# Performance work log

Measured on AMD Instinct MI355X. Metric: run time of the kernel, lower is better.

The kernel has to match this reference:

```python
import jax, jax.numpy as jnp
import numpy as np

B, L, H, R = 8, 8256, 768, 24  # L = 128*129/2 flattened token-pair positions


def setup_inputs() -> dict:
    key = jax.random.key(0)
    k1, k2, k3 = jax.random.split(key, 3)
    hidden_state = jax.random.normal(k1, (B, L, H), dtype=jnp.float32)
    # per-relation Linear(hidden_size, 3) weights, stacked: (R, 3, H), (R, 3)
    W = jax.random.normal(k2, (R, 3, H), dtype=jnp.float32) * 0.02
    b = jax.random.normal(k3, (R, 3), dtype=jnp.float32) * 0.02
    return {"hidden_state": hidden_state, "W": W, "b": b}


def reference(hidden_state, W, b):
    # Batched equivalent of the per-relation Linear loop + stack(dim=1):
    # logits[b, r, l, t] = sum_h hidden_state[b,l,h] * W[r,t,h] + b[r,t]
    logits = jnp.einsum('blh,rth->brlt', hidden_state, W) + b[None, :, None, :]
    return jax.nn.softmax(logits, axis=-1)  # (B, R, L, 3)
```

## Files before the change

kernel.cpp:

```cpp
#include <hip/hip_runtime.h>
#include <hip/hip_bf16.h>


#define HD     768
#define LSEQ   8256
#define RREL   24
#define KSTEPS 24
#define NT     5
#define NCOL   72
#define MF     4

typedef float f32x4 __attribute__((ext_vector_type(4)));
typedef short s16x8 __attribute__((ext_vector_type(8)));
typedef int   i32x4 __attribute__((ext_vector_type(4)));

__device__ __forceinline__ unsigned f2bf_rne(float f) {
  unsigned u = __builtin_bit_cast(unsigned, f);
  u += 0x7FFFu + ((u >> 16) & 1u);
  return u >> 16;
}

__device__ __forceinline__ int pack2(float lo, float hi) {
  unsigned l = __bfloat16_as_ushort(__float2bfloat16(lo));
  unsigned h = __bfloat16_as_ushort(__float2bfloat16(hi));
  return (int)(l | (h << 16));
}

__global__ void conv_w_kernel(const float* __restrict__ W,
                              unsigned short* __restrict__ wsB) {
  int idx = blockIdx.x * 256 + threadIdx.x;
  if (idx >= KSTEPS * NT * 64) return;
  int ks   = idx / (NT * 64);
  int rem  = idx - ks * (NT * 64);
  int nt   = rem >> 6;
  int lane = rem & 63;
  int col  = nt * 16 + (lane & 15);
  int k0   = ks * 32 + (lane >> 4) * 8;
  unsigned short v[8] = {0, 0, 0, 0, 0, 0, 0, 0};
  if (col < NCOL) {
    const float* p = W + (size_t)col * HD + k0;
    float4 a = *(const float4*)p;
    float4 b = *(const float4*)(p + 4);
    v[0] = (unsigned short)f2bf_rne(a.x); v[1] = (unsigned short)f2bf_rne(a.y);
    v[2] = (unsigned short)f2bf_rne(a.z); v[3] = (unsigned short)f2bf_rne(a.w);
    v[4] = (unsigned short)f2bf_rne(b.x); v[5] = (unsigned short)f2bf_rne(b.y);
    v[6] = (unsigned short)f2bf_rne(b.z); v[7] = (unsigned short)f2bf_rne(b.w);
  }
  *(s16x8*)(wsB + (size_t)idx * 8) = *(s16x8*)v;
}

#define ALOAD4(ks) do { if ((ks) < KSTEPS) {                       \
    const int s_ = (ks) % 3, o_ = (ks) * 32;                       \
    _Pragma("unroll")                                              \
    for (int ph_ = 0; ph_ < MF; ++ph_) {                           \
      abuf[s_][ph_][0] = *(const float4*)(pA[ph_] + o_);           \
      abuf[s_][ph_][1] = *(const float4*)(pA[ph_] + o_ + 4);       \
    }                                                              \
  } } while (0)

#define BLOAD4(ks) do { if ((ks) < KSTEPS) {                       \
    _Pragma("unroll")                                              \
    for (int nt_ = 0; nt_ < NT; ++nt_)                             \
      bbuf[(ks) & 1][nt_] = pWS[(ks) * NT * 64 + nt_ * 64 + lane]; \
  } } while (0)

__global__ __launch_bounds__(64, 1)
void tagging_m64(const float* __restrict__ hs, const float* __restrict__ bias,
                 const i32x4* __restrict__ pWS, float* __restrict__ out) {
  __shared__ float lg[64][85];

  const int lane = threadIdx.x;
  const int m0   = blockIdx.x * 64;

  const float* pA[MF];
  #pragma unroll
  for (int ph = 0; ph < MF; ++ph)
    pA[ph] = hs + (size_t)(m0 + ph * 16 + (lane >> 2)) * HD + (lane & 3) * 8;
  const int bp = ((lane & 15) * 4 + (lane >> 4)) * 4;

  f32x4  acc[MF][NT] = {};
  float4 abuf[3][MF][2];
  i32x4  bbuf[2][NT];

  ALOAD4(0); ALOAD4(1);
  BLOAD4(0);

  #pragma unroll
  for (int ks = 0; ks < KSTEPS; ++ks) {
    ALOAD4(ks + 2);
    BLOAD4(ks + 1);

    s16x8 af[MF];
    #pragma unroll
    for (int mt = 0; mt < MF; ++mt) {
      float4 a0 = abuf[ks % 3][mt][0], a1 = abuf[ks % 3][mt][1];
      i32x4 av;
      av[0] = __builtin_amdgcn_ds_bpermute(bp, pack2(a0.x, a0.y));
      av[1] = __builtin_amdgcn_ds_bpermute(bp, pack2(a0.z, a0.w));
      av[2] = __builtin_amdgcn_ds_bpermute(bp, pack2(a1.x, a1.y));
      av[3] = __builtin_amdgcn_ds_bpermute(bp, pack2(a1.z, a1.w));
      af[mt] = __builtin_bit_cast(s16x8, av);
    }

    #pragma unroll
    for (int nt = 0; nt < NT; ++nt) {
      s16x8 bf = __builtin_bit_cast(s16x8, bbuf[ks & 1][nt]);
      #pragma unroll
      for (int mt = 0; mt < MF; ++mt)
        acc[mt][nt] = __builtin_amdgcn_mfma_f32_16x16x32_bf16(af[mt], bf, acc[mt][nt], 0, 0, 0);
    }
  }

  #pragma unroll
  for (int mt = 0; mt < MF; ++mt)
    #pragma unroll
    for (int nt = 0; nt < NT; ++nt)
      #pragma unroll
      for (int j = 0; j < 4; ++j)
        lg[mt * 16 + (lane >> 4) * 4 + j][nt * 16 + (lane & 15)] = acc[mt][nt][j];
  __syncthreads();

  const int bidx = m0 / LSEQ;
  const int l0   = m0 - bidx * LSEQ;
  #pragma unroll
  for (int it = 0; it < 24; ++it) {
    const int g    = it;
    const int tokl = lane;
    float x0 = lg[tokl][3 * g + 0] + bias[3 * g + 0];
    float x1 = lg[tokl][3 * g + 1] + bias[3 * g + 1];
    float x2 = lg[tokl][3 * g + 2] + bias[3 * g + 2];
    float mx = fmaxf(x0, fmaxf(x1, x2));
    float e0 = __expf(x0 - mx), e1 = __expf(x1 - mx), e2 = __expf(x2 - mx);
    float inv = 1.0f / (e0 + e1 + e2);
    size_t o = ((size_t)(bidx * RREL + g) * LSEQ + l0 + tokl) * 3;
    out[o + 0] = e0 * inv;
    out[o + 1] = e1 * inv;
    out[o + 2] = e2 * inv;
  }
}

__global__ __launch_bounds__(64, 2)
void tagging_fb(const float* __restrict__ hs, const float* __restrict__ W,
                const float* __restrict__ bias, float* __restrict__ out) {
  __shared__ float lg[32][85];
  const int lane = threadIdx.x;
  const int m0   = blockIdx.x * 32;

  const float* pA0 = hs + (size_t)(m0 + (lane >> 2)) * HD + (lane & 3) * 8;
  const float* pA1 = pA0 + 16 * HD;
  const int bp = ((lane & 15) * 4 + (lane >> 4)) * 4;

  const float* pB[NT];
  #pragma unroll
  for (int nt = 0; nt < NT; ++nt)
    pB[nt] = W + (size_t)(nt * 16 + (lane & 15)) * HD + (lane >> 4) * 8;
  const bool b4ok = (lane & 15) < 8;

  f32x4  acc[2][NT] = {};
  float4 abuf[3][2][2];
  float4 fbf[2][NT][2];

#define FB_ALOAD(ks) do { if ((ks) < KSTEPS) {                     \
    const int s_ = (ks) % 3, o_ = (ks) * 32;                       \
    abuf[s_][0][0] = *(const float4*)(pA0 + o_);                   \
    abuf[s_][0][1] = *(const float4*)(pA0 + o_ + 4);               \
    abuf[s_][1][0] = *(const float4*)(pA1 + o_);                   \
    abuf[s_][1][1] = *(const float4*)(pA1 + o_ + 4);               \
  } } while (0)

#define FB_BLOAD(ks) do { if ((ks) < KSTEPS) {                     \
    _Pragma("unroll")                                              \
    for (int nt_ = 0; nt_ < 4; ++nt_) {                            \
      fbf[(ks) & 1][nt_][0] = *(const float4*)(pB[nt_] + (ks)*32); \
      fbf[(ks) & 1][nt_][1] = *(const float4*)(pB[nt_] + (ks)*32 + 4); \
    }                                                              \
    if (b4ok) {                                                    \
      fbf[(ks) & 1][4][0] = *(const float4*)(pB[4] + (ks)*32);     \
      fbf[(ks) & 1][4][1] = *(const float4*)(pB[4] + (ks)*32 + 4); \
    } else {                                                       \
      fbf[(ks) & 1][4][0] = make_float4(0.f,0.f,0.f,0.f);          \
      fbf[(ks) & 1][4][1] = make_float4(0.f,0.f,0.f,0.f);          \
    }                                                              \
  } } while (0)

  FB_ALOAD(0); FB_ALOAD(1);
  FB_BLOAD(0);

  #pragma unroll
  for (int ks = 0; ks < KSTEPS; ++ks) {
    FB_ALOAD(ks + 2);
    FB_BLOAD(ks + 1);
    s16x8 af[2];
    #pragma unroll
    for (int mt = 0; mt < 2; ++mt) {
      float4 a0 = abuf[ks % 3][mt][0], a1 = abuf[ks % 3][mt][1];
      i32x4 av;
      av[0] = __builtin_amdgcn_ds_bpermute(bp, pack2(a0.x, a0.y));
      av[1] = __builtin_amdgcn_ds_bpermute(bp, pack2(a0.z, a0.w));
      av[2] = __builtin_amdgcn_ds_bpermute(bp, pack2(a1.x, a1.y));
      av[3] = __builtin_amdgcn_ds_bpermute(bp, pack2(a1.z, a1.w));
      af[mt] = __builtin_bit_cast(s16x8, av);
    }
    #pragma unroll
    for (int nt = 0; nt < NT; ++nt) {
      float4 b0 = fbf[ks & 1][nt][0], b1 = fbf[ks & 1][nt][1];
      i32x4 bv;
      bv[0] = pack2(b0.x, b0.y); bv[1] = pack2(b0.z, b0.w);
      bv[2] = pack2(b1.x, b1.y); bv[3] = pack2(b1.z, b1.w);
      s16x8 bf = __builtin_bit_cast(s16x8, bv);
      acc[0][nt] = __builtin_amdgcn_mfma_f32_16x16x32_bf16(af[0], bf, acc[0][nt], 0, 0, 0);
      acc[1][nt] = __builtin_amdgcn_mfma_f32_16x16x32_bf16(af[1], bf, acc[1][nt], 0, 0, 0);
    }
  }

  #pragma unroll
  for (int mt = 0; mt < 2; ++mt)
    #pragma unroll
    for (int nt = 0; nt < NT; ++nt)
      #pragma unroll
      for (int j = 0; j < 4; ++j)
        lg[mt * 16 + (lane >> 4) * 4 + j][nt * 16 + (lane & 15)] = acc[mt][nt][j];
  __syncthreads();

  const int bidx = m0 / LSEQ;
  const int l0   = m0 - bidx * LSEQ;
  #pragma unroll
  for (int it = 0; it < 12; ++it) {
    int flat = it * 64 + lane;
    int g    = flat >> 5;
    int tokl = flat & 31;
    float x0 = lg[tokl][3 * g + 0] + bias[3 * g + 0];
    float x1 = lg[tokl][3 * g + 1] + bias[3 * g + 1];
    float x2 = lg[tokl][3 * g + 2] + bias[3 * g + 2];
    float mx = fmaxf(x0, fmaxf(x1, x2));
    float e0 = __expf(x0 - mx), e1 = __expf(x1 - mx), e2 = __expf(x2 - mx);
    float inv = 1.0f / (e0 + e1 + e2);
    size_t o = ((size_t)(bidx * RREL + g) * LSEQ + l0 + tokl) * 3;
    out[o + 0] = e0 * inv;
    out[o + 1] = e1 * inv;
    out[o + 2] = e2 * inv;
  }
}

extern "C" void kernel_launch(void* const* d_in, const int* in_sizes, int n_in,
                              void* d_out, int out_size, void* d_ws, size_t ws_size,
                              hipStream_t stream) {
  (void)in_sizes; (void)n_in; (void)out_size;
  const float* hs   = (const float*)d_in[0];
  const float* W    = (const float*)d_in[1];
  const float* bias = (const float*)d_in[2];
  float* out = (float*)d_out;

  const size_t needB = (size_t)KSTEPS * NT * 64 * 8 * 2;
  if (d_ws && ws_size >= needB) {
    hipLaunchKernelGGL(conv_w_kernel, dim3(30), dim3(256), 0, stream,
                       W, (unsigned short*)d_ws);
    hipLaunchKernelGGL(tagging_m64, dim3(1032), dim3(64), 0, stream,
                       hs, bias, (const i32x4*)d_ws, out);
  } else {
    hipLaunchKernelGGL(tagging_fb, dim3(2064), dim3(64), 0, stream,
                       hs, W, bias, out);
  }
}
```

Baseline: 48.81 us.

## Shrink main GEMM tile to 32 rows, triple-buffer B, pin schedule groups

The main kernel now uses 32-row tiles per 64-thread block instead of 64 rows, doubling the grid to 2064 blocks and allowing two blocks per CU via launch bounds. The B fragments from workspace are triple-buffered and prefetched two steps ahead, and explicit sched_group_barrier hints interleave VMEM loads, VALU packing, ds_bpermute and MFMA. The softmax epilogue is remapped so 64 lanes cover 32 tokens across relation groups. Smaller tiles lower register pressure and raise occupancy, but they also reload the B operand twice as often.

```diff
diff --git a/kernel.cpp b/kernel.cpp
--- a/kernel.cpp
+++ b/kernel.cpp
@@ -8,7 +8,6 @@
 #define KSTEPS 24
 #define NT     5
 #define NCOL   72
-#define MF     4
 
 typedef float f32x4 __attribute__((ext_vector_type(4)));
 typedef short s16x8 __attribute__((ext_vector_type(8)));
@@ -49,50 +48,51 @@
   *(s16x8*)(wsB + (size_t)idx * 8) = *(s16x8*)v;
 }
 
-#define ALOAD4(ks) do { if ((ks) < KSTEPS) {                       \
+#define ALOAD(ks) do { if ((ks) < KSTEPS) {                        \
     const int s_ = (ks) % 3, o_ = (ks) * 32;                       \
-    _Pragma("unroll")                                              \
-    for (int ph_ = 0; ph_ < MF; ++ph_) {                           \
-      abuf[s_][ph_][0] = *(const float4*)(pA[ph_] + o_);           \
-      abuf[s_][ph_][1] = *(const float4*)(pA[ph_] + o_ + 4);       \
-    }                                                              \
+    abuf[s_][0][0] = *(const float4*)(pA0 + o_);                   \
+    abuf[s_][0][1] = *(const float4*)(pA0 + o_ + 4);               \
+    abuf[s_][1][0] = *(const float4*)(pA1 + o_);                   \
+    abuf[s_][1][1] = *(const float4*)(pA1 + o_ + 4);               \
   } } while (0)
 
-#define BLOAD4(ks) do { if ((ks) < KSTEPS) {                       \
+#define BLOAD_WS(ks) do { if ((ks) < KSTEPS) {                     \
     _Pragma("unroll")                                              \
     for (int nt_ = 0; nt_ < NT; ++nt_)                             \
-      bbuf[(ks) & 1][nt_] = pWS[(ks) * NT * 64 + nt_ * 64 + lane]; \
+      bbuf[(ks) % 3][nt_] = pWS[(ks) * NT * 64 + nt_ * 64 + lane]; \
   } } while (0)
 
-__global__ __launch_bounds__(64, 1)
-void tagging_m64(const float* __restrict__ hs, const float* __restrict__ bias,
+__global__ __launch_bounds__(64, 2)
+void tagging_pin(const float* __restrict__ hs, const float* __restrict__ bias,
                  const i32x4* __restrict__ pWS, float* __restrict__ out) {
-  __shared__ float lg[64][85];
+  __shared__ float lg[32][85];
 
   const int lane = threadIdx.x;
-  const int m0   = blockIdx.x * 64;
-
-  const float* pA[MF];
-  #pragma unroll
-  for (int ph = 0; ph < MF; ++ph)
-    pA[ph] = hs + (size_t)(m0 + ph * 16 + (lane >> 2)) * HD + (lane & 3) * 8;
+  const int m0   = blockIdx.x * 32;
+
+  const float* pA0 = hs + (size_t)(m0 + (lane >> 2)) * HD + (lane & 3) * 8;
+  const float* pA1 = pA0 + 16 * HD;
   const int bp = ((lane & 15) * 4 + (lane >> 4)) * 4;
 
-  f32x4  acc[MF][NT] = {};
-  float4 abuf[3][MF][2];
-  i32x4  bbuf[2][NT];
-
-  ALOAD4(0); ALOAD4(1);
-  BLOAD4(0);
+  f32x4  acc[2][NT] = {};
+  float4 abuf[3][2][2];
+  i32x4  bbuf[3][NT];
+
+  BLOAD_WS(0); BLOAD_WS(1);
+  ALOAD(0); ALOAD(1);
 
   #pragma unroll
   for (int ks = 0; ks < KSTEPS; ++ks) {
-    ALOAD4(ks + 2);
-    BLOAD4(ks + 1);
-
-    s16x8 af[MF];
-    #pragma unroll
-    for (int mt = 0; mt < MF; ++mt) {
+    BLOAD_WS(ks + 2);
+    ALOAD(ks + 2);
+    __builtin_amdgcn_sched_group_barrier(0x020, 9, 0);
+    __builtin_amdgcn_sched_group_barrier(0x002, 16, 0);
+    __builtin_amdgcn_sched_group_barrier(0x180, 8, 0);
+    __builtin_amdgcn_sched_group_barrier(0x008, 10, 0);
+
+    s16x8 af[2];
+    #pragma unroll
+    for (int mt = 0; mt < 2; ++mt) {
       float4 a0 = abuf[ks % 3][mt][0], a1 = abuf[ks % 3][mt][1];
       i32x4 av;
       av[0] = __builtin_amdgcn_ds_bpermute(bp, pack2(a0.x, a0.y));
@@ -104,15 +104,14 @@
 
     #pragma unroll
     for (int nt = 0; nt < NT; ++nt) {
-      s16x8 bf = __builtin_bit_cast(s16x8, bbuf[ks & 1][nt]);
-      #pragma unroll
-      for (int mt = 0; mt < MF; ++mt)
-        acc[mt][nt] = __builtin_amdgcn_mfma_f32_16x16x32_bf16(af[mt], bf, acc[mt][nt], 0, 0, 0);
-    }
-  }
-
-  #pragma unroll
-  for (int mt = 0; mt < MF; ++mt)
+      s16x8 bf = __builtin_bit_cast(s16x8, bbuf[ks % 3][nt]);
+      acc[0][nt] = __builtin_amdgcn_mfma_f32_16x16x32_bf16(af[0], bf, acc[0][nt], 0, 0, 0);
+      acc[1][nt] = __builtin_amdgcn_mfma_f32_16x16x32_bf16(af[1], bf, acc[1][nt], 0, 0, 0);
+    }
+  }
+
+  #pragma unroll
+  for (int mt = 0; mt < 2; ++mt)
     #pragma unroll
     for (int nt = 0; nt < NT; ++nt)
       #pragma unroll
@@ -123,9 +122,10 @@
   const int bidx = m0 / LSEQ;
   const int l0   = m0 - bidx * LSEQ;
   #pragma unroll
-  for (int it = 0; it < 24; ++it) {
-    const int g    = it;
-    const int tokl = lane;
+  for (int it = 0; it < 12; ++it) {
+    int flat = it * 64 + lane;
+    int g    = flat >> 5;
+    int tokl = flat & 31;
     float x0 = lg[tokl][3 * g + 0] + bias[3 * g + 0];
     float x1 = lg[tokl][3 * g + 1] + bias[3 * g + 1];
     float x2 = lg[tokl][3 * g + 2] + bias[3 * g + 2];
@@ -159,14 +159,6 @@
   f32x4  acc[2][NT] = {};
   float4 abuf[3][2][2];
   float4 fbf[2][NT][2];
-
-#define FB_ALOAD(ks) do { if ((ks) < KSTEPS) {                     \
-    const int s_ = (ks) % 3, o_ = (ks) * 32;                       \
-    abuf[s_][0][0] = *(const float4*)(pA0 + o_);                   \
-    abuf[s_][0][1] = *(const float4*)(pA0 + o_ + 4);               \
-    abuf[s_][1][0] = *(const float4*)(pA1 + o_);                   \
-    abuf[s_][1][1] = *(const float4*)(pA1 + o_ + 4);               \
-  } } while (0)
 
 #define FB_BLOAD(ks) do { if ((ks) < KSTEPS) {                     \
     _Pragma("unroll")                                              \
@@ -183,13 +175,13 @@
     }                                                              \
   } } while (0)
 
-  FB_ALOAD(0); FB_ALOAD(1);
   FB_BLOAD(0);
+  ALOAD(0); ALOAD(1);
 
   #pragma unroll
   for (int ks = 0; ks < KSTEPS; ++ks) {
-    FB_ALOAD(ks + 2);
     FB_BLOAD(ks + 1);
+    ALOAD(ks + 2);
     s16x8 af[2];
     #pragma unroll
     for (int mt = 0; mt < 2; ++mt) {
@@ -255,7 +247,7 @@
   if (d_ws && ws_size >= needB) {
     hipLaunchKernelGGL(conv_w_kernel, dim3(30), dim3(256), 0, stream,
                        W, (unsigned short*)d_ws);
-    hipLaunchKernelGGL(tagging_m64, dim3(1032), dim3(64), 0, stream,
+    hipLaunchKernelGGL(tagging_pin, dim3(2064), dim3(64), 0, stream,
                        hs, bias, (const i32x4*)d_ws, out);
   } else {
     hipLaunchKernelGGL(tagging_fb, dim3(2064), dim3(64), 0, stream,
```

Result: slower. 57.97 us (+18.8%).
